# Kernel optimization log

Hardware: AMD Instinct MI355X
Metric: run time of the kernel (lower is better)

## Reference

```python
import jax, jax.numpy as jnp
import numpy as np

IN_CH, OUT_CH, K, POOL = 3, 16, 3, 2

def setup_inputs() -> dict:
    key = jax.random.key(0)
    kx, kw, kb = jax.random.split(key, 3)
    B, H, W = 64, 512, 512
    x = jax.random.normal(kx, (B, IN_CH, H, W), dtype=jnp.float32)
    fan_in = IN_CH * K * K
    bound = 1.0 / np.sqrt(fan_in)
    weight = jax.random.uniform(kw, (OUT_CH, IN_CH, K, K), dtype=jnp.float32, minval=-bound, maxval=bound)
    bias = jax.random.uniform(kb, (OUT_CH,), dtype=jnp.float32, minval=-bound, maxval=bound)
    return {"x": x, "weight": weight, "bias": bias}

def reference(x, weight, bias):
    # Conv2d, stride 1, VALID padding (matches in_h - k + 1 in kernel)
    y = jax.lax.conv_general_dilated(
        x, weight, window_strides=(1, 1), padding="VALID",
        dimension_numbers=("NCHW", "OIHW", "NCHW"))
    y = y + bias[None, :, None, None]  # [B, OC, Hc, Wc]
    B, C, Hc, Wc = y.shape
    Hp, Wp = Hc // POOL, Wc // POOL
    # Average pool 2x2 (floor-cropped like the CUDA kernel's integer division)
    y = y[:, :, :Hp * POOL, :Wp * POOL].reshape(B, C, Hp, POOL, Wp, POOL).mean(axis=(3, 5))
    # Sigmoid then sum over channel + spatial dims -> one scalar per batch element
    return jax.nn.sigmoid(y).sum(axis=(1, 2, 3))
```

## Files before the change

kernel.cpp:

```cpp
#include <hip/hip_runtime.h>


#define IC 3
#define OCH 16
#define HH 512
#define WW 512
#define HP 255
#define SROWS 5
#define STRIPS 51

typedef float v2f __attribute__((ext_vector_type(2)));

__device__ __forceinline__ float fast_sigmoid(float v) {
    float e = __expf(-v);
    return __builtin_amdgcn_rcpf(1.0f + e);
}

__global__ void build_weff(const float* __restrict__ w,
                           const float* __restrict__ bias,
                           float* __restrict__ ws)
{
    const int i = threadIdx.x;
    for (int idx = i; idx < OCH * 48; idx += 256) {
        int oc = idx / 48;
        int rem = idx - oc * 48;
        int ic = rem >> 4;
        int ky = (rem >> 2) & 3;
        int kx = rem & 3;
        float s = 0.f;
#pragma unroll
        for (int py = 0; py < 2; ++py) {
            int r = ky - py;
            if (r < 0 || r > 2) continue;
#pragma unroll
            for (int px = 0; px < 2; ++px) {
                int c = kx - px;
                if (c < 0 || c > 2) continue;
                s += w[((oc * IC + ic) * 3 + r) * 3 + c];
            }
        }
        ws[oc * 64 + rem] = 0.25f * s;
    }
    if (i < OCH) ws[i * 64 + 48] = bias[i];
}

__global__ __launch_bounds__(128)
void conv_pool_sig_sum(const float* __restrict__ x,
                       const float* __restrict__ wws,
                       float* __restrict__ out)
{
    const int tid = threadIdx.x;
    const bool v1 = (tid < 127);
    const int c0 = 4 * tid;
    const int b = blockIdx.y;
    const int hp0 = blockIdx.x * SROWS;
    const int tail = v1 ? 4 : 0;

    const float* xb = x + ((size_t)b * IC * HH + (size_t)2 * hp0) * WW + c0;

    float lsum = 0.f, lsum1 = 0.f;

    for (int s = 0; s < SROWS; ++s) {
        float4 xa[IC][4];
        float2 xt[IC][4];
#pragma unroll
        for (int ic = 0; ic < IC; ++ic) {
            const float* pr = xb + (size_t)ic * HH * WW;
#pragma unroll
            for (int r = 0; r < 4; ++r) {
                xa[ic][r] = *(const float4*)(pr + r * WW);
                xt[ic][r] = *(const float2*)(pr + r * WW + tail);
            }
        }

#pragma unroll 1
        for (int oc = 0; oc < OCH; ++oc) {
            const float* we = wws + oc * 64;
            const float bv = we[48];
            v2f acc = {bv, bv};
#pragma unroll
            for (int ic = 0; ic < IC; ++ic) {
#pragma unroll
                for (int r = 0; r < 4; ++r) {
                    const float4 a = xa[ic][r];
                    const float2 t = xt[ic][r];
                    const float* wr = we + ic * 16 + r * 4;
                    acc += (v2f){a.x, a.z} * wr[0];
                    acc += (v2f){a.y, a.w} * wr[1];
                    acc += (v2f){a.z, t.x} * wr[2];
                    acc += (v2f){a.w, t.y} * wr[3];
                }
            }
            lsum  += fast_sigmoid(acc.x);
            lsum1 += fast_sigmoid(acc.y);
        }
        xb += 2 * WW;
    }
    lsum += v1 ? lsum1 : 0.f;

#pragma unroll
    for (int off = 32; off > 0; off >>= 1)
        lsum += __shfl_xor(lsum, off, 64);
    if ((tid & 63) == 0) atomicAdd(out + b, lsum);
}

extern "C" void kernel_launch(void* const* d_in, const int* in_sizes, int n_in,
                              void* d_out, int out_size, void* d_ws, size_t ws_size,
                              hipStream_t stream) {
    const float* x = (const float*)d_in[0];
    const float* w = (const float*)d_in[1];
    const float* bias = (const float*)d_in[2];
    float* out = (float*)d_out;
    float* wws = (float*)d_ws;

    hipMemsetAsync(out, 0, out_size * sizeof(float), stream);
    build_weff<<<1, 256, 0, stream>>>(w, bias, wws);

    dim3 grid(STRIPS, 64);
    conv_pool_sig_sum<<<grid, 128, 0, stream>>>(x, wws, out);
}
```

Baseline: 334.2 us.

## Restructure conv-pool as rolling row pipeline with per-thread all-channel accumulators

Each thread now owns one pooled output column and slides down the strip row by row. All 16 output channels are held as accumulators, and each input row pair is applied to two adjacent pooled rows through split weight tables. This means every input row is loaded once per strip instead of twice for overlapping windows, and rows are prefetched while the taps of the current row are computed. Block size doubles to 256 with a new weight table layout. The cost is much higher register pressure (32 accumulators plus buffers) and some wasted lanes at the edge.

Measured after the change: 405.1 us. 1.21x slower.

```diff
diff --git a/kernel.cpp b/kernel.cpp
--- a/kernel.cpp
+++ b/kernel.cpp
@@ -5,8 +5,8 @@
 #define OCH 16
 #define HH 512
 #define WW 512
-#define HP 255
-#define SROWS 5
+#define WP 255
+#define L 5
 #define STRIPS 51
 
 typedef float v2f __attribute__((ext_vector_type(2)));
@@ -21,82 +21,113 @@
                            float* __restrict__ ws)
 {
     const int i = threadIdx.x;
-    for (int idx = i; idx < OCH * 48; idx += 256) {
-        int oc = idx / 48;
-        int rem = idx - oc * 48;
-        int ic = rem >> 4;
-        int ky = (rem >> 2) & 3;
-        int kx = rem & 3;
-        float s = 0.f;
+    for (int idx = i; idx < 384; idx += 256) {
+        const int oc  = idx & 15;
+        const int tap = idx >> 4;
+        const int kx  = tap & 3;
+        const int t2  = tap >> 2;
+        const int kyp = t2 / 3;
+        const int ic  = t2 - kyp * 3;
+        float s[2];
 #pragma unroll
-        for (int py = 0; py < 2; ++py) {
-            int r = ky - py;
-            if (r < 0 || r > 2) continue;
+        for (int which = 0; which < 2; ++which) {
+            const int ky = which ? kyp : kyp + 2;
+            float acc = 0.f;
 #pragma unroll
-            for (int px = 0; px < 2; ++px) {
-                int c = kx - px;
-                if (c < 0 || c > 2) continue;
-                s += w[((oc * IC + ic) * 3 + r) * 3 + c];
+            for (int py = 0; py < 2; ++py) {
+                int r = ky - py;
+                if (r < 0 || r > 2) continue;
+#pragma unroll
+                for (int px = 0; px < 2; ++px) {
+                    int c = kx - px;
+                    if (c < 0 || c > 2) continue;
+                    acc += w[((oc * IC + ic) * 3 + r) * 3 + c];
+                }
             }
+            s[which] = 0.25f * acc;
         }
-        ws[oc * 64 + rem] = 0.25f * s;
+        ws[2 * idx]     = s[0];
+        ws[2 * idx + 1] = s[1];
     }
-    if (i < OCH) ws[i * 64 + 48] = bias[i];
+    if (i < OCH) ws[768 + i] = bias[i];
 }
 
-__global__ __launch_bounds__(128)
+#define LOADROW(buf, q)                                                  \
+    {                                                                    \
+        _Pragma("unroll")                                                \
+        for (int ic_ = 0; ic_ < IC; ++ic_) {                             \
+            const float* p_ = xb + (size_t)ic_ * (HH * WW)               \
+                                 + (size_t)(q) * WW;                     \
+            buf[ic_][0] = *(const v2f*)p_;                               \
+            buf[ic_][1] = *(const v2f*)(p_ + 2);                         \
+        }                                                                \
+    }
+
+#define TAPS(buf, kyp)                                                   \
+    {                                                                    \
+        _Pragma("unroll")                                                \
+        for (int ic_ = 0; ic_ < IC; ++ic_) {                             \
+            _Pragma("unroll")                                            \
+            for (int kx_ = 0; kx_ < 4; ++kx_) {                          \
+                const float xv_ = (kx_ < 2) ? buf[ic_][0][kx_]           \
+                                            : buf[ic_][1][kx_ - 2];      \
+                const v2f* wp_ = wtab + (((kyp) * IC + ic_) * 4 + kx_) * 16; \
+                _Pragma("unroll")                                        \
+                for (int oc_ = 0; oc_ < OCH; ++oc_)                      \
+                    acc[oc_] += wp_[oc_] * xv_;                          \
+            }                                                            \
+        }                                                                \
+    }
+
+__global__ __launch_bounds__(256, 4)
 void conv_pool_sig_sum(const float* __restrict__ x,
-                       const float* __restrict__ wws,
+                       const float* __restrict__ ws,
                        float* __restrict__ out)
 {
     const int tid = threadIdx.x;
-    const bool v1 = (tid < 127);
-    const int c0 = 4 * tid;
+    const int j = (tid < WP) ? tid : WP - 1;
     const int b = blockIdx.y;
-    const int hp0 = blockIdx.x * SROWS;
-    const int tail = v1 ? 4 : 0;
+    const int r0 = blockIdx.x * L;
 
-    const float* xb = x + ((size_t)b * IC * HH + (size_t)2 * hp0) * WW + c0;
+    const v2f* __restrict__ wtab = (const v2f*)ws;
+    const float* __restrict__ bs = ws + 768;
 
-    float lsum = 0.f, lsum1 = 0.f;
+    const float* xb = x + (size_t)b * IC * HH * WW
+                        + (size_t)(2 * r0) * WW + 2 * j;
 
-    for (int s = 0; s < SROWS; ++s) {
-        float4 xa[IC][4];
-        float2 xt[IC][4];
+    v2f xA[IC][2], xB[IC][2];
+    LOADROW(xA, 0)
+    LOADROW(xB, 1)
+
+    v2f acc[OCH];
 #pragma unroll
-        for (int ic = 0; ic < IC; ++ic) {
-            const float* pr = xb + (size_t)ic * HH * WW;
+    for (int oc = 0; oc < OCH; ++oc) acc[oc] = (v2f){0.f, 0.f};
+
+    float lsum = 0.f;
+
+#pragma unroll 1
+    for (int t = 0; t <= L; ++t) {
 #pragma unroll
-            for (int r = 0; r < 4; ++r) {
-                xa[ic][r] = *(const float4*)(pr + r * WW);
-                xt[ic][r] = *(const float2*)(pr + r * WW + tail);
-            }
+        for (int oc = 0; oc < OCH; ++oc) {
+            acc[oc].x = acc[oc].y;
+            acc[oc].y = bs[oc];
         }
 
-#pragma unroll 1
-        for (int oc = 0; oc < OCH; ++oc) {
-            const float* we = wws + oc * 64;
-            const float bv = we[48];
-            v2f acc = {bv, bv};
+        TAPS(xA, 0)
+        { const int qa = (2 * t + 2 <= 2 * L + 1) ? (2 * t + 2) : (2 * L + 1);
+          LOADROW(xA, qa) }
+
+        TAPS(xB, 1)
+        { const int qb = (2 * t + 3 <= 2 * L + 1) ? (2 * t + 3) : (2 * L + 1);
+          LOADROW(xB, qb) }
+
+        if (t > 0) {
 #pragma unroll
-            for (int ic = 0; ic < IC; ++ic) {
-#pragma unroll
-                for (int r = 0; r < 4; ++r) {
-                    const float4 a = xa[ic][r];
-                    const float2 t = xt[ic][r];
-                    const float* wr = we + ic * 16 + r * 4;
-                    acc += (v2f){a.x, a.z} * wr[0];
-                    acc += (v2f){a.y, a.w} * wr[1];
-                    acc += (v2f){a.z, t.x} * wr[2];
-                    acc += (v2f){a.w, t.y} * wr[3];
-                }
-            }
-            lsum  += fast_sigmoid(acc.x);
-            lsum1 += fast_sigmoid(acc.y);
+            for (int oc = 0; oc < OCH; ++oc) lsum += fast_sigmoid(acc[oc].x);
         }
-        xb += 2 * WW;
     }
-    lsum += v1 ? lsum1 : 0.f;
+
+    if (tid >= WP) lsum = 0.f;
 
 #pragma unroll
     for (int off = 32; off > 0; off >>= 1)
@@ -117,5 +148,5 @@
     build_weff<<<1, 256, 0, stream>>>(w, bias, wws);
 
     dim3 grid(STRIPS, 64);
-    conv_pool_sig_sum<<<grid, 128, 0, stream>>>(x, wws, out);
+    conv_pool_sig_sum<<<grid, 256, 0, stream>>>(x, wws, out);
 }
```

## Stream input row pairs through double-buffered LDS and reuse across pooled rows

Applied to the files above, without the earlier changes.

Each block now walks a strip of 15 pooled rows, loading only two new input rows per step into a double-buffered shared-memory buffer. Per-channel accumulators for adjacent pooled rows are carried over, so each input row is read from global memory once instead of twice. Global loads for the next step are issued before the compute on the current buffer to overlap latency. In exchange, register pressure rises from 32 live accumulators, there is one barrier per step, and the grid is smaller, which lowers parallelism.

Measured after the change: 404.4 us. 21.0% more time.

```diff
diff --git a/kernel.cpp b/kernel.cpp
--- a/kernel.cpp
+++ b/kernel.cpp
@@ -5,11 +5,13 @@
 #define OCH 16
 #define HH 512
 #define WW 512
-#define HP 255
-#define SROWS 5
-#define STRIPS 51
+#define WP 255
+#define L 15
+#define STRIPS 17
+#define RSTRIDE 520
 
 typedef float v2f __attribute__((ext_vector_type(2)));
+typedef float v4f __attribute__((ext_vector_type(4)));
 
 __device__ __forceinline__ float fast_sigmoid(float v) {
     float e = __expf(-v);
@@ -22,86 +24,134 @@
 {
     const int i = threadIdx.x;
     for (int idx = i; idx < OCH * 48; idx += 256) {
-        int oc = idx / 48;
-        int rem = idx - oc * 48;
-        int ic = rem >> 4;
-        int ky = (rem >> 2) & 3;
-        int kx = rem & 3;
+        const int oc = idx / 48;
+        const int r  = idx - oc * 48;
+        const int kx = r & 3;
+        const int t2 = r >> 2;
+        const int ky = t2 / 3;
+        const int ic = t2 - ky * 3;
         float s = 0.f;
 #pragma unroll
         for (int py = 0; py < 2; ++py) {
-            int r = ky - py;
-            if (r < 0 || r > 2) continue;
+            int rr = ky - py;
+            if (rr < 0 || rr > 2) continue;
 #pragma unroll
             for (int px = 0; px < 2; ++px) {
-                int c = kx - px;
-                if (c < 0 || c > 2) continue;
-                s += w[((oc * IC + ic) * 3 + r) * 3 + c];
+                int cc = kx - px;
+                if (cc < 0 || cc > 2) continue;
+                s += w[((oc * IC + ic) * 3 + rr) * 3 + cc];
             }
         }
-        ws[oc * 64 + rem] = 0.25f * s;
+        ws[oc * 64 + r] = 0.25f * s;
     }
     if (i < OCH) ws[i * 64 + 48] = bias[i];
 }
 
-__global__ __launch_bounds__(128)
+__global__ __launch_bounds__(128, 3)
 void conv_pool_sig_sum(const float* __restrict__ x,
                        const float* __restrict__ wws,
                        float* __restrict__ out)
 {
     const int tid = threadIdx.x;
-    const bool v1 = (tid < 127);
-    const int c0 = 4 * tid;
-    const int b = blockIdx.y;
-    const int hp0 = blockIdx.x * SROWS;
-    const int tail = v1 ? 4 : 0;
+    const int b   = blockIdx.y;
+    const int r0  = blockIdx.x * L;
 
-    const float* xb = x + ((size_t)b * IC * HH + (size_t)2 * hp0) * WW + c0;
+    __shared__ float sbuf[2][2 * IC * RSTRIDE];
+    __shared__ float red[2];
 
-    float lsum = 0.f, lsum1 = 0.f;
+    const float* xg = x + (size_t)b * (IC * HH * WW) + 4 * tid;
 
-    for (int s = 0; s < SROWS; ++s) {
-        float4 xa[IC][4];
-        float2 xt[IC][4];
+    {
+        v4f st[6];
 #pragma unroll
-        for (int ic = 0; ic < IC; ++ic) {
-            const float* pr = xb + (size_t)ic * HH * WW;
+        for (int pl = 0; pl < 6; ++pl) {
+            const int r = pl / 3, ic = pl - 3 * r;
+            st[pl] = *(const v4f*)(xg + (size_t)ic * (HH * WW)
+                                      + (size_t)(2 * r0 + r) * WW);
+        }
 #pragma unroll
-            for (int r = 0; r < 4; ++r) {
-                xa[ic][r] = *(const float4*)(pr + r * WW);
-                xt[ic][r] = *(const float2*)(pr + r * WW + tail);
+        for (int pl = 0; pl < 6; ++pl)
+            *(v4f*)(&sbuf[0][pl * RSTRIDE + 4 * tid]) = st[pl];
+    }
+    __syncthreads();
+
+    v2f ao[OCH], an[OCH];
+#pragma unroll
+    for (int oc = 0; oc < OCH; ++oc) an[oc] = (v2f){0.f, 0.f};
+    float lsA = 0.f, lsB = 0.f;
+
+#pragma unroll 1
+    for (int t = 0; t <= L; ++t) {
+        const int pp = t & 1;
+
+        v4f st[6];
+        const bool dost = (t < L);
+        if (dost) {
+#pragma unroll
+            for (int pl = 0; pl < 6; ++pl) {
+                const int r = pl / 3, ic = pl - 3 * r;
+                st[pl] = *(const v4f*)(xg + (size_t)ic * (HH * WW)
+                                          + (size_t)(2 * r0 + 2 * t + 2 + r) * WW);
             }
         }
 
-#pragma unroll 1
+        v2f xv[2][IC][4];
+#pragma unroll
+        for (int par = 0; par < 2; ++par)
+#pragma unroll
+            for (int ic = 0; ic < IC; ++ic) {
+                const float* p = &sbuf[pp][(par * IC + ic) * RSTRIDE + 4 * tid];
+                const v4f a  = *(const v4f*)p;
+                const v4f bq = *(const v4f*)(p + 4);
+                xv[par][ic][0] = (v2f){a.x, a.z};
+                xv[par][ic][1] = (v2f){a.y, a.w};
+                xv[par][ic][2] = (v2f){a.z, bq.x};
+                xv[par][ic][3] = (v2f){a.w, bq.y};
+            }
+
+#pragma unroll
         for (int oc = 0; oc < OCH; ++oc) {
             const float* we = wws + oc * 64;
+            ao[oc] = an[oc];
             const float bv = we[48];
-            v2f acc = {bv, bv};
+            an[oc] = (v2f){bv, bv};
 #pragma unroll
-            for (int ic = 0; ic < IC; ++ic) {
+            for (int par = 0; par < 2; ++par)
 #pragma unroll
-                for (int r = 0; r < 4; ++r) {
-                    const float4 a = xa[ic][r];
-                    const float2 t = xt[ic][r];
-                    const float* wr = we + ic * 16 + r * 4;
-                    acc += (v2f){a.x, a.z} * wr[0];
-                    acc += (v2f){a.y, a.w} * wr[1];
-                    acc += (v2f){a.z, t.x} * wr[2];
-                    acc += (v2f){a.w, t.y} * wr[3];
-                }
+                for (int ic = 0; ic < IC; ++ic)
+#pragma unroll
+                    for (int kx = 0; kx < 4; ++kx) {
+                        const v2f xvv = xv[par][ic][kx];
+                        ao[oc] += xvv * we[((par + 2) * IC + ic) * 4 + kx];
+                        an[oc] += xvv * we[(par * IC + ic) * 4 + kx];
+                    }
+        }
+
+        if (t > 0) {
+#pragma unroll
+            for (int oc = 0; oc < OCH; ++oc) {
+                lsA += fast_sigmoid(ao[oc].x);
+                lsB += fast_sigmoid(ao[oc].y);
             }
-            lsum  += fast_sigmoid(acc.x);
-            lsum1 += fast_sigmoid(acc.y);
         }
-        xb += 2 * WW;
+
+        if (dost) {
+#pragma unroll
+            for (int pl = 0; pl < 6; ++pl)
+                *(v4f*)(&sbuf[pp ^ 1][pl * RSTRIDE + 4 * tid]) = st[pl];
+        }
+        __syncthreads();
     }
-    lsum += v1 ? lsum1 : 0.f;
+
+    if (2 * tid + 1 >= WP) lsB = 0.f;
+    float lsum = lsA + lsB;
 
 #pragma unroll
     for (int off = 32; off > 0; off >>= 1)
         lsum += __shfl_xor(lsum, off, 64);
-    if ((tid & 63) == 0) atomicAdd(out + b, lsum);
+    if ((tid & 63) == 0) red[tid >> 6] = lsum;
+    __syncthreads();
+    if (tid == 0) atomicAdd(out + b, red[0] + red[1]);
 }
 
 extern "C" void kernel_launch(void* const* d_in, const int* in_sizes, int n_in,
```

## Stream input rows once with ping-pong pooled-row accumulators and split output channels

Applied to the files above, without the earlier changes.

The kernel now walks each strip one input row pair at a time. Every loaded row feeds two rolling accumulator sets, for the current and next pooled row, so each input row is loaded once per block instead of twice. Output channels are split into two chunks of eight across blockIdx.x, and the effective weights are re-laid out per chunk and row parity. The grid becomes 2x64x17 blocks with 15 pooled rows each, and the atomic is reduced to one per block through shared memory. In exchange, each input is read by two channel-chunk blocks, register pressure rises from the unrolled accumulators, and the grid has fewer blocks, which may lower occupancy.

Result: slower. 445.4 us (+33.3%).

```diff
diff --git a/kernel.cpp b/kernel.cpp
--- a/kernel.cpp
+++ b/kernel.cpp
@@ -3,13 +3,12 @@
 
 #define IC 3
 #define OCH 16
+#define OCC 8
 #define HH 512
 #define WW 512
-#define HP 255
-#define SROWS 5
-#define STRIPS 51
-
-typedef float v2f __attribute__((ext_vector_type(2)));
+#define WP 255
+#define L 15
+#define STRIPS 17
 
 __device__ __forceinline__ float fast_sigmoid(float v) {
     float e = __expf(-v);
@@ -21,87 +20,115 @@
                            float* __restrict__ ws)
 {
     const int i = threadIdx.x;
-    for (int idx = i; idx < OCH * 48; idx += 256) {
-        int oc = idx / 48;
-        int rem = idx - oc * 48;
-        int ic = rem >> 4;
-        int ky = (rem >> 2) & 3;
-        int kx = rem & 3;
+    for (int idx = i; idx < 768; idx += 256) {
+        const int blk   = idx >> 6;
+        const int r     = idx & 63;
+        const int oc8   = r >> 3;
+        const int which = (r >> 2) & 1;
+        const int kx    = r & 3;
+        const int ic    = blk % 3;
+        const int t2    = blk / 3;
+        const int par   = t2 & 1;
+        const int chunk = t2 >> 1;
+        const int oc    = chunk * OCC + oc8;
+        const int ky    = which ? par : (par + 2);
         float s = 0.f;
 #pragma unroll
         for (int py = 0; py < 2; ++py) {
-            int r = ky - py;
-            if (r < 0 || r > 2) continue;
+            int rr = ky - py;
+            if (rr < 0 || rr > 2) continue;
 #pragma unroll
             for (int px = 0; px < 2; ++px) {
-                int c = kx - px;
-                if (c < 0 || c > 2) continue;
-                s += w[((oc * IC + ic) * 3 + r) * 3 + c];
+                int cc = kx - px;
+                if (cc < 0 || cc > 2) continue;
+                s += w[((oc * IC + ic) * 3 + rr) * 3 + cc];
             }
         }
-        ws[oc * 64 + rem] = 0.25f * s;
+        ws[idx] = 0.25f * s;
     }
-    if (i < OCH) ws[i * 64 + 48] = bias[i];
+    if (i < OCH) ws[768 + i] = bias[i];
 }
+
+#define STEP(T, AO, AN, EMIT)                                               \
+  {                                                                         \
+    _Pragma("unroll")                                                       \
+    for (int par = 0; par < 2; ++par) {                                     \
+      _Pragma("unroll")                                                     \
+      for (int ic = 0; ic < IC; ++ic) {                                     \
+        const float* xp = xg + (size_t)ic * (HH * WW)                       \
+                             + (size_t)(2 * (T) + par) * WW;                \
+        const float4 a  = *(const float4*)xp;                               \
+        const float2 tv = *(const float2*)(xp + tail);                      \
+        const float xB2 = tv.x, xB3 = tv.y;                                 \
+        const float* wb = wbase + (par * IC + ic) * 64;                     \
+        _Pragma("unroll")                                                   \
+        for (int o = 0; o < OCC; ++o) {                                     \
+          const float wo0 = wb[o*8+0], wo1 = wb[o*8+1];                     \
+          const float wo2 = wb[o*8+2], wo3 = wb[o*8+3];                     \
+          const float wn0 = wb[o*8+4], wn1 = wb[o*8+5];                     \
+          const float wn2 = wb[o*8+6], wn3 = wb[o*8+7];                     \
+          AO[o][0] += a.x*wo0 + a.y*wo1 + a.z*wo2 + a.w*wo3;                \
+          AO[o][1] += a.z*wo0 + a.w*wo1 + xB2*wo2 + xB3*wo3;                \
+          AN[o][0] += a.x*wn0 + a.y*wn1 + a.z*wn2 + a.w*wn3;                \
+          AN[o][1] += a.z*wn0 + a.w*wn1 + xB2*wn2 + xB3*wn3;                \
+        }                                                                   \
+      }                                                                     \
+    }                                                                       \
+    if (EMIT) {                                                             \
+      _Pragma("unroll")                                                     \
+      for (int o = 0; o < OCC; ++o) {                                       \
+        lsA += fast_sigmoid(AO[o][0]);                                      \
+        lsB += fast_sigmoid(AO[o][1]);                                      \
+      }                                                                     \
+    }                                                                       \
+    _Pragma("unroll")                                                       \
+    for (int o = 0; o < OCC; ++o) { AO[o][0] = bv[o]; AO[o][1] = bv[o]; }   \
+  }
 
 __global__ __launch_bounds__(128)
 void conv_pool_sig_sum(const float* __restrict__ x,
                        const float* __restrict__ wws,
                        float* __restrict__ out)
 {
-    const int tid = threadIdx.x;
-    const bool v1 = (tid < 127);
-    const int c0 = 4 * tid;
-    const int b = blockIdx.y;
-    const int hp0 = blockIdx.x * SROWS;
-    const int tail = v1 ? 4 : 0;
+    const int tid   = threadIdx.x;
+    const int chunk = blockIdx.x;
+    const int b     = blockIdx.y;
+    const int r0    = blockIdx.z * L;
+    const int tail  = (tid < 127) ? 4 : 0;
 
-    const float* xb = x + ((size_t)b * IC * HH + (size_t)2 * hp0) * WW + c0;
+    const float* xg = x + (size_t)b * (IC * HH * WW)
+                        + (size_t)(2 * r0) * WW + 4 * tid;
+    const float* wbase = wws + chunk * (2 * IC * 64);
 
-    float lsum = 0.f, lsum1 = 0.f;
+    float bv[OCC];
+#pragma unroll
+    for (int o = 0; o < OCC; ++o) bv[o] = wws[768 + chunk * OCC + o];
 
-    for (int s = 0; s < SROWS; ++s) {
-        float4 xa[IC][4];
-        float2 xt[IC][4];
+    float aX[OCC][2], aY[OCC][2];
 #pragma unroll
-        for (int ic = 0; ic < IC; ++ic) {
-            const float* pr = xb + (size_t)ic * HH * WW;
-#pragma unroll
-            for (int r = 0; r < 4; ++r) {
-                xa[ic][r] = *(const float4*)(pr + r * WW);
-                xt[ic][r] = *(const float2*)(pr + r * WW + tail);
-            }
-        }
+    for (int o = 0; o < OCC; ++o) {
+        aX[o][0] = bv[o]; aX[o][1] = bv[o];
+        aY[o][0] = bv[o]; aY[o][1] = bv[o];
+    }
+    float lsA = 0.f, lsB = 0.f;
 
 #pragma unroll 1
-        for (int oc = 0; oc < OCH; ++oc) {
-            const float* we = wws + oc * 64;
-            const float bv = we[48];
-            v2f acc = {bv, bv};
-#pragma unroll
-            for (int ic = 0; ic < IC; ++ic) {
-#pragma unroll
-                for (int r = 0; r < 4; ++r) {
-                    const float4 a = xa[ic][r];
-                    const float2 t = xt[ic][r];
-                    const float* wr = we + ic * 16 + r * 4;
-                    acc += (v2f){a.x, a.z} * wr[0];
-                    acc += (v2f){a.y, a.w} * wr[1];
-                    acc += (v2f){a.z, t.x} * wr[2];
-                    acc += (v2f){a.w, t.y} * wr[3];
-                }
-            }
-            lsum  += fast_sigmoid(acc.x);
-            lsum1 += fast_sigmoid(acc.y);
-        }
-        xb += 2 * WW;
+    for (int t = 0; t < L; t += 2) {
+        STEP(t,     aX, aY, (t > 0))
+        STEP(t + 1, aY, aX, true)
     }
-    lsum += v1 ? lsum1 : 0.f;
+
+    if (2 * tid + 1 >= WP) lsB = 0.f;
+    float lsum = lsA + lsB;
 
 #pragma unroll
     for (int off = 32; off > 0; off >>= 1)
         lsum += __shfl_xor(lsum, off, 64);
-    if ((tid & 63) == 0) atomicAdd(out + b, lsum);
+
+    __shared__ float red[2];
+    if ((tid & 63) == 0) red[tid >> 6] = lsum;
+    __syncthreads();
+    if (tid == 0) atomicAdd(out + b, red[0] + red[1]);
 }
 
 extern "C" void kernel_launch(void* const* d_in, const int* in_sizes, int n_in,
@@ -116,6 +143,6 @@
     hipMemsetAsync(out, 0, out_size * sizeof(float), stream);
     build_weff<<<1, 256, 0, stream>>>(w, bias, wws);
 
-    dim3 grid(STRIPS, 64);
+    dim3 grid(2, 64, STRIPS);
     conv_pool_sig_sum<<<grid, 128, 0, stream>>>(x, wws, out);
 }
```
